# Optimization experiments

Measured on AMD Instinct MI355X. Metric: run time of the kernel, lower is better.

## Reference

```python
import jax, jax.numpy as jnp
import numpy as np

ATTRIBUTE_NUMS = [3, 3, 1, 4, 3]
WINDOW_SIZE = 10


def setup_inputs() -> dict:
    key = jax.random.key(0)
    ks = jax.random.split(key, 7)
    b, s, n_l, f = 4, 2048, 4, 64
    A, L = 14, 5  # num_attributes, levels per attribute
    scale_tensor = jax.random.normal(ks[0], (b, s, n_l, f), dtype=jnp.float32)
    scale = 1.0 / np.sqrt(f).astype(np.float32)
    Wq = jax.random.normal(ks[1], (A, L, f, f), dtype=jnp.float32) * scale
    bq = jax.random.normal(ks[2], (A, L, f), dtype=jnp.float32) * 0.01
    Wk = jax.random.normal(ks[3], (A, L, f, f), dtype=jnp.float32) * scale
    bk = jax.random.normal(ks[4], (A, L, f), dtype=jnp.float32) * 0.01
    Wt = jax.random.normal(ks[5], (A, L, f, f), dtype=jnp.float32) * scale
    bt = jax.random.normal(ks[6], (A, L, f), dtype=jnp.float32) * 0.01
    return {"scale_tensor": scale_tensor, "Wq": Wq, "bq": bq, "Wk": Wk,
            "bk": bk, "Wt": Wt, "bt": bt, "scale_idx": 4}


def reference(scale_tensor, Wq, bq, Wk, bk, Wt, bt, scale_idx):
    b, s, a, f = scale_tensor.shape
    k = WINDOW_SIZE * (6 - scale_idx)  # half window (static python int)
    w = 2 * k + 1
    l_i = scale_idx
    off = sum(ATTRIBUTE_NUMS[:scale_idx - 1])
    # select the parameters actually used: attributes [off, off+a), levels [0, l_i)
    Wq_s, bq_s = Wq[off:off + a, :l_i], bq[off:off + a, :l_i]  # [a,l,f,f], [a,l,f]
    Wk_s, bk_s = Wk[off:off + a, :l_i], bk[off:off + a, :l_i]
    Wt_s, bt_s = Wt[off:off + a, :l_i], bt[off:off + a, :l_i]

    # sliding windows over the sequence axis (zero-padded), shared across levels
    padded = jnp.pad(scale_tensor, ((0, 0), (k, k), (0, 0), (0, 0)))
    idx = jnp.arange(s)[:, None] + jnp.arange(w)[None, :]  # [s, w]
    win = padded[:, idx]                                   # [b,s,w,a,f]
    zero_mask = jnp.all(win == 0, axis=-1)                 # [b,s,w,a]

    # queries: q = x @ Wq^T + bq  (torch Linear convention, W is [out,in])
    q = jnp.einsum('bsaf,algf->bsalg', scale_tensor, Wq_s) + bq_s  # [b,s,a,l,f]
    qk = jnp.einsum('bsalg,algf->bsalf', q, Wk_s)                  # [b,s,a,l,f]
    attn = jnp.einsum('bsalf,bswaf->bsalw', qk, win)
    attn = attn + jnp.einsum('bsalg,alg->bsal', q, bk_s)[..., None]
    attn = attn / np.float32(np.sqrt(f))

    mask = jnp.transpose(zero_mask, (0, 1, 3, 2))[:, :, :, None, :]  # [b,s,a,1,w]
    attn = jnp.where(mask, jnp.float32(-1e9), attn)
    wgt = jax.nn.softmax(attn, axis=-1)                    # [b,s,a,l,w]

    ctx = jnp.einsum('bsalw,bswaf->bsalf', wgt, win)       # [b,s,a,l,f]
    out = jnp.einsum('bsalf,algf->bsalg', ctx, Wt_s) + bt_s
    return out  # [b,s,a,l_i,f]
```

## Files before the change

### kernel.cpp

```cpp
#include <hip/hip_runtime.h>
#include <hip/hip_bf16.h>

#define SDIM 2048
#define ADIM 4
#define KWIN 20
#define WWIN 41
#define CHUNK 64

typedef __attribute__((ext_vector_type(8))) short s8v;
typedef __attribute__((ext_vector_type(4))) float f32x4;
#define MFMA __builtin_amdgcn_mfma_f32_16x16x32_bf16

#define WSB_MB 8256
#define WSB_WT 172096

#define O_YJF 0
#define O_YFJ 16128
#define O_B1  31488
#define O_CTX 40704
#define O_RF  49920
#define LDS_TOTAL 50368

__device__ __forceinline__ int detect_is_bf16(const void* xp) {
  const unsigned* w = (const unsigned*)xp;
  const unsigned word = w[threadIdx.x & 63];
  const unsigned e = (word >> 7) & 0xFFu;
  const unsigned long long m = __ballot(e >= 118u && e <= 132u);
  return __popcll(m) >= 32;
}
__device__ __forceinline__ float ldf(const void* p, size_t i, int isbf) {
  return isbf ? __bfloat162float(((const __hip_bfloat16*)p)[i]) : ((const float*)p)[i];
}
__device__ __forceinline__ s8v ld8l(const char* p) { return *(const s8v*)p; }
__device__ __forceinline__ s8v ld8g(const short* p) { return *(const s8v*)p; }

__global__ __launch_bounds__(256) void prep_kernel(
    const void* __restrict__ x,
    const void* __restrict__ Wq, const void* __restrict__ bq,
    const void* __restrict__ Wk, const void* __restrict__ bk,
    const void* __restrict__ Wt, const void* __restrict__ bt,
    const int* __restrict__ sip, float* __restrict__ ws) {
  const int isbf = detect_is_bf16(x);
  const int al = blockIdx.x, a = al >> 2, li = al & 3;
  const int si = *sip;
  int off = 0;
  const int ATTR[5] = {3, 3, 1, 4, 3};
  for (int i = 0; i < si - 1 && i < 5; ++i) off += ATTR[i];
  const size_t wb = ((size_t)(off + a) * 5 + li) * 4096;
  const size_t bb = ((size_t)(off + a) * 5 + li) * 64;
  const int tid = threadIdx.x;

  __shared__ float sq[4096], sk[4096];
  __shared__ float sbq[64], sbk[64];
  for (int i = tid; i < 4096; i += 256) {
    sq[i] = ldf(Wq, wb + i, isbf);
    sk[i] = ldf(Wk, wb + i, isbf);
  }
  if (tid < 64) { sbq[tid] = ldf(bq, bb + tid, isbf); sbk[tid] = ldf(bk, bb + tid, isbf); }
  __syncthreads();

  __hip_bfloat16* mb  = (__hip_bfloat16*)((char*)ws + WSB_MB) + (size_t)al * 5120;
  __hip_bfloat16* wtb = (__hip_bfloat16*)((char*)ws + WSB_WT) + (size_t)al * 4096;

  for (int i = tid; i < 4096; i += 256) {
    const int f = i >> 6, f2 = i & 63;
    float acc = 0.f;
    #pragma unroll 16
    for (int g = 0; g < 64; ++g) acc += sk[g * 64 + f] * sq[g * 64 + f2];
    mb[f * 64 + f2] = __float2bfloat16(acc);
    wtb[i] = __float2bfloat16(ldf(Wt, wb + i, isbf));
  }
  if (tid < 64) {
    float u = 0.f, v = 0.f;
    for (int g = 0; g < 64; ++g) {
      u += sq[g * 64 + tid] * sbk[g];
      v += sk[g * 64 + tid] * sbq[g];
    }
    mb[64 * 64 + tid] = __float2bfloat16(u);
    ws[al * 64 + tid] = v;
    ws[1024 + al * 64 + tid] = ldf(bt, bb + tid, isbf);
  }
  for (int i = tid; i < 15 * 64; i += 256) mb[65 * 64 + i] = __float2bfloat16(0.f);
  if (tid == 0) {
    float c = 0.f;
    for (int g = 0; g < 64; ++g) c += sbq[g] * sbk[g];
    ws[2048 + al] = c;
  }
}

__global__ __launch_bounds__(256) void attn_kernel(
    const void* __restrict__ x, const float* __restrict__ ws,
    float* __restrict__ out) {
  const int isbf = detect_is_bf16(x);
  const int chunk = blockIdx.x;
  const int ba = blockIdx.y;
  const int b = ba >> 2, a = ba & 3;
  const int s0 = chunk * CHUNK;
  const int tid = threadIdx.x;
  const int lane = tid & 63;
  const int mt = tid >> 6;
  const int c16 = lane & 15;
  const int q = lane >> 4;

  __shared__ __align__(16) char lds[LDS_TOTAL];

  for (int r = mt; r < 112; r += 4) {
    const int j = s0 - KWIN + r;
    float yv = 0.f;
    if (r < 104 && j >= 0 && j < SDIM)
      yv = ldf(x, (((size_t)b * SDIM + j) * ADIM + a) * 64 + lane, isbf);
    const __hip_bfloat16 hv = __float2bfloat16(yv);
    *(__hip_bfloat16*)(lds + O_YJF + r * 144 + lane * 2) = hv;
    *(__hip_bfloat16*)(lds + O_YFJ + lane * 240 + r * 2) = hv;
    const unsigned long long nz = __ballot(yv != 0.f);
    if (lane == 0) ((float*)(lds + O_RF))[r] = nz ? 1.f : 0.f;
  }
  __syncthreads();

  const short* mbase  = (const short*)((const char*)ws + WSB_MB);
  const short* wtbase = (const short*)((const char*)ws + WSB_WT);

  const char* xr = lds + O_YJF + (KWIN + 16 * mt + c16) * 144 + q * 16;
  const s8v xa0 = ld8l(xr), xa1 = ld8l(xr + 64);
  float rfv[4];
  #pragma unroll
  for (int nt = 0; nt < 4; ++nt)
    rfv[nt] = ((const float*)(lds + O_RF))[16 * mt + nt * 16 + c16];

  for (int l = 0; l < 4; ++l) {
    const int al = a * 4 + l;
    const short* mb  = mbase + (size_t)al * 5120;
    const short* wtb = wtbase + (size_t)al * 4096;
    const float c_al = ws[2048 + al];

    f32x4 uacc;
    #pragma unroll
    for (int nt = 0; nt < 5; ++nt) {
      const int n = nt * 16 + c16;
      const s8v b0 = ld8g(mb + n * 64 + q * 8);
      const s8v b1 = ld8g(mb + n * 64 + 32 + q * 8);
      const float vv = (nt < 4) ? ws[al * 64 + n] : 0.f;
      f32x4 acc = {vv, vv, vv, vv};
      acc = MFMA(xa0, b0, acc, 0, 0, 0);
      acc = MFMA(xa1, b1, acc, 0, 0, 0);
      if (nt < 4) {
        #pragma unroll
        for (int r = 0; r < 4; ++r)
          *(__hip_bfloat16*)(lds + O_B1 + (16 * mt + 4 * q + r) * 144 + n * 2) =
              __float2bfloat16(acc[r]);
      } else {
        uacc = acc;
      }
    }
    float uxr[4];
    #pragma unroll
    for (int r = 0; r < 4; ++r) uxr[r] = __shfl(uacc[r], lane & 48) + c_al;
    __threadfence_block();

    const char* qrow = lds + O_B1 + (16 * mt + c16) * 144 + q * 16;
    const s8v qa0 = ld8l(qrow), qa1 = ld8l(qrow + 64);
    f32x4 sacc[4];
    #pragma unroll
    for (int nt = 0; nt < 4; ++nt) {
      const char* yr = lds + O_YJF + (16 * mt + nt * 16 + c16) * 144 + q * 16;
      const s8v b0 = ld8l(yr), b1 = ld8l(yr + 64);
      f32x4 s = {0.f, 0.f, 0.f, 0.f};
      s = MFMA(qa0, b0, s, 0, 0, 0);
      s = MFMA(qa1, b1, s, 0, 0, 0);
      sacc[nt] = s;
    }

    float ee[4][4];
    float mx[4] = {-3.0e38f, -3.0e38f, -3.0e38f, -3.0e38f};
    #pragma unroll
    for (int nt = 0; nt < 4; ++nt) {
      const int jl = nt * 16 + c16;
      #pragma unroll
      for (int r = 0; r < 4; ++r) {
        const int w = jl - (4 * q + r);
        float lv = -1.0e9f;
        if (w >= 0 && w < WWIN && rfv[nt] != 0.f)
          lv = (sacc[nt][r] + uxr[r]) * 0.125f;
        ee[nt][r] = lv;
        mx[r] = fmaxf(mx[r], lv);
      }
    }
    #pragma unroll
    for (int r = 0; r < 4; ++r) {
      #pragma unroll
      for (int o = 1; o < 16; o <<= 1) mx[r] = fmaxf(mx[r], __shfl_xor(mx[r], o));
    }
    float se[4] = {0.f, 0.f, 0.f, 0.f};
    #pragma unroll
    for (int nt = 0; nt < 4; ++nt)
      #pragma unroll
      for (int r = 0; r < 4; ++r) {
        const float e = __expf(ee[nt][r] - mx[r]);
        ee[nt][r] = e;
        se[r] += e;
      }
    float rse[4];
    #pragma unroll
    for (int r = 0; r < 4; ++r) {
      #pragma unroll
      for (int o = 1; o < 16; o <<= 1) se[r] += __shfl_xor(se[r], o);
      rse[r] = 1.f / se[r];
    }
    #pragma unroll
    for (int nt = 0; nt < 4; ++nt)
      #pragma unroll
      for (int r = 0; r < 4; ++r)
        *(__hip_bfloat16*)(lds + O_B1 + (16 * mt + 4 * q + r) * 144 +
                           (nt * 16 + c16) * 2) = __float2bfloat16(ee[nt][r]);
    __threadfence_block();

    const char* prow = lds + O_B1 + (16 * mt + c16) * 144 + q * 16;
    const s8v pa0 = ld8l(prow), pa1 = ld8l(prow + 64);
    #pragma unroll
    for (int nt = 0; nt < 4; ++nt) {
      const int f = nt * 16 + c16;
      const char* brow = lds + O_YFJ + f * 240 + 32 * mt + q * 16;
      const s8v b0 = ld8l(brow), b1 = ld8l(brow + 64);
      f32x4 cc = {0.f, 0.f, 0.f, 0.f};
      cc = MFMA(pa0, b0, cc, 0, 0, 0);
      cc = MFMA(pa1, b1, cc, 0, 0, 0);
      #pragma unroll
      for (int r = 0; r < 4; ++r)
        *(__hip_bfloat16*)(lds + O_CTX + (16 * mt + 4 * q + r) * 144 + f * 2) =
            __float2bfloat16(cc[r] * rse[r]);
    }
    __threadfence_block();

    const char* crow = lds + O_CTX + (16 * mt + c16) * 144 + q * 16;
    const s8v ca0 = ld8l(crow), ca1 = ld8l(crow + 64);
    #pragma unroll
    for (int nt = 0; nt < 4; ++nt) {
      const int g = nt * 16 + c16;
      const s8v b0 = ld8g(wtb + g * 64 + q * 8);
      const s8v b1 = ld8g(wtb + g * 64 + 32 + q * 8);
      f32x4 o = {0.f, 0.f, 0.f, 0.f};
      o = MFMA(ca0, b0, o, 0, 0, 0);
      o = MFMA(ca1, b1, o, 0, 0, 0);
      const float btv = ws[1024 + al * 64 + g];
      #pragma unroll
      for (int r = 0; r < 4; ++r) {
        const int row = 16 * mt + 4 * q + r;
        const size_t idx =
            (((size_t)b * SDIM + (s0 + row)) * ADIM + a) * 256 + l * 64 + g;
        out[idx] = o[r] + btv;
      }
    }
  }
}

extern "C" void kernel_launch(void* const* d_in, const int* in_sizes, int n_in,
                              void* d_out, int out_size, void* d_ws, size_t ws_size,
                              hipStream_t stream) {
  const void* x  = d_in[0];
  const void* Wq = d_in[1];
  const void* bq = d_in[2];
  const void* Wk = d_in[3];
  const void* bk = d_in[4];
  const void* Wt = d_in[5];
  const void* bt = d_in[6];
  const int* sip = (const int*)d_in[7];
  float* ws = (float*)d_ws;
  float* out = (float*)d_out;

  prep_kernel<<<16, 256, 0, stream>>>(x, Wq, bq, Wk, bk, Wt, bt, sip, ws);
  attn_kernel<<<dim3(SDIM / CHUNK, 16), 256, 0, stream>>>(x, ws, out);
}
```

Before: 137.2 us.

## Keep attention intermediates in registers via transposed MFMA and lane shuffles

The attention kernel swaps MFMA operand order so each result tile comes out transposed, then rebuilds the next MFMA's operand with cross-lane shuffles instead of bouncing q, probabilities and context through LDS. This removes the B1/CTX scratch regions and their LDS round-trips, cutting LDS size. It also splits levels across a new grid z-dimension for more blocks, vectorizes the input and output accesses with float4, and spreads the prep kernel over four blocks per (attribute, level). The cost is extra shuffle instructions and some duplicated x staging across the two level-halves.

```diff
diff --git a/kernel.cpp b/kernel.cpp
--- a/kernel.cpp
+++ b/kernel.cpp
@@ -2,10 +2,8 @@
 #include <hip/hip_bf16.h>
 
 #define SDIM 2048
-#define ADIM 4
 #define KWIN 20
 #define WWIN 41
-#define CHUNK 64
 
 typedef __attribute__((ext_vector_type(8))) short s8v;
 typedef __attribute__((ext_vector_type(4))) float f32x4;
@@ -16,10 +14,8 @@
 
 #define O_YJF 0
 #define O_YFJ 16128
-#define O_B1  31488
-#define O_CTX 40704
-#define O_RF  49920
-#define LDS_TOTAL 50368
+#define O_RF  31488
+#define LDS_TOTAL 31936
 
 __device__ __forceinline__ int detect_is_bf16(const void* xp) {
   const unsigned* w = (const unsigned*)xp;
@@ -31,8 +27,29 @@
 __device__ __forceinline__ float ldf(const void* p, size_t i, int isbf) {
   return isbf ? __bfloat162float(((const __hip_bfloat16*)p)[i]) : ((const float*)p)[i];
 }
-__device__ __forceinline__ s8v ld8l(const char* p) { return *(const s8v*)p; }
-__device__ __forceinline__ s8v ld8g(const short* p) { return *(const s8v*)p; }
+__device__ __forceinline__ unsigned bfb(float f) {
+  union { float f; unsigned u; } x; x.f = f;
+  return (x.u + 0x7FFFu + ((x.u >> 16) & 1u)) >> 16;
+}
+__device__ __forceinline__ int pkbf(float a, float b) {
+  return (int)(bfb(a) | (bfb(b) << 16));
+}
+__device__ __forceinline__ s8v xform(int p00, int p01, int p10, int p11, int lane) {
+  const int q = lane >> 4;
+  const int sA = (lane & 15) + ((q & 1) << 5);
+  const int sB = sA + 16;
+  const bool hi = (q >> 1) != 0;
+  const int w0a = __shfl(p00, sA), w0b = __shfl(p10, sA);
+  const int w1a = __shfl(p01, sA), w1b = __shfl(p11, sA);
+  const int w2a = __shfl(p00, sB), w2b = __shfl(p10, sB);
+  const int w3a = __shfl(p01, sB), w3b = __shfl(p11, sB);
+  union { int i[4]; s8v v; } u;
+  u.i[0] = hi ? w0b : w0a;
+  u.i[1] = hi ? w1b : w1a;
+  u.i[2] = hi ? w2b : w2a;
+  u.i[3] = hi ? w3b : w3a;
+  return u.v;
+}
 
 __global__ __launch_bounds__(256) void prep_kernel(
     const void* __restrict__ x,
@@ -42,6 +59,7 @@
     const int* __restrict__ sip, float* __restrict__ ws) {
   const int isbf = detect_is_bf16(x);
   const int al = blockIdx.x, a = al >> 2, li = al & 3;
+  const int fq = blockIdx.y;
   const int si = *sip;
   int off = 0;
   const int ATTR[5] = {3, 3, 1, 4, 3};
@@ -62,40 +80,43 @@
   __hip_bfloat16* mb  = (__hip_bfloat16*)((char*)ws + WSB_MB) + (size_t)al * 5120;
   __hip_bfloat16* wtb = (__hip_bfloat16*)((char*)ws + WSB_WT) + (size_t)al * 4096;
 
-  for (int i = tid; i < 4096; i += 256) {
-    const int f = i >> 6, f2 = i & 63;
+  for (int t = tid; t < 1024; t += 256) {
+    const int f = fq * 16 + (t >> 6), f2 = t & 63;
     float acc = 0.f;
     #pragma unroll 16
     for (int g = 0; g < 64; ++g) acc += sk[g * 64 + f] * sq[g * 64 + f2];
     mb[f * 64 + f2] = __float2bfloat16(acc);
-    wtb[i] = __float2bfloat16(ldf(Wt, wb + i, isbf));
-  }
-  if (tid < 64) {
-    float u = 0.f, v = 0.f;
-    for (int g = 0; g < 64; ++g) {
-      u += sq[g * 64 + tid] * sbk[g];
-      v += sk[g * 64 + tid] * sbq[g];
-    }
-    mb[64 * 64 + tid] = __float2bfloat16(u);
-    ws[al * 64 + tid] = v;
-    ws[1024 + al * 64 + tid] = ldf(bt, bb + tid, isbf);
-  }
-  for (int i = tid; i < 15 * 64; i += 256) mb[65 * 64 + i] = __float2bfloat16(0.f);
-  if (tid == 0) {
-    float c = 0.f;
-    for (int g = 0; g < 64; ++g) c += sbq[g] * sbk[g];
-    ws[2048 + al] = c;
-  }
-}
-
-__global__ __launch_bounds__(256) void attn_kernel(
+    wtb[f * 64 + f2] = __float2bfloat16(ldf(Wt, wb + f * 64 + f2, isbf));
+  }
+  if (fq == 0) {
+    if (tid < 64) {
+      float u = 0.f, v = 0.f;
+      for (int g = 0; g < 64; ++g) {
+        u += sq[g * 64 + tid] * sbk[g];
+        v += sk[g * 64 + tid] * sbq[g];
+      }
+      mb[64 * 64 + tid] = __float2bfloat16(u);
+      ws[al * 64 + tid] = v;
+      ws[1024 + al * 64 + tid] = ldf(bt, bb + tid, isbf);
+    }
+    for (int i = tid; i < 15 * 64; i += 256) mb[65 * 64 + i] = __float2bfloat16(0.f);
+    if (tid == 0) {
+      float c = 0.f;
+      for (int g = 0; g < 64; ++g) c += sbq[g] * sbk[g];
+      ws[2048 + al] = c;
+    }
+  }
+}
+
+__global__ __launch_bounds__(256, 4) void attn_kernel(
     const void* __restrict__ x, const float* __restrict__ ws,
     float* __restrict__ out) {
   const int isbf = detect_is_bf16(x);
   const int chunk = blockIdx.x;
   const int ba = blockIdx.y;
+  const int lp = blockIdx.z;
   const int b = ba >> 2, a = ba & 3;
-  const int s0 = chunk * CHUNK;
+  const int s0 = chunk * 64;
   const int tid = threadIdx.x;
   const int lane = tid & 63;
   const int mt = tid >> 6;
@@ -104,151 +125,149 @@
 
   __shared__ __align__(16) char lds[LDS_TOTAL];
 
-  for (int r = mt; r < 112; r += 4) {
+  #pragma unroll
+  for (int it = 0; it < 7; ++it) {
+    const int r = it * 16 + (tid >> 4);
     const int j = s0 - KWIN + r;
-    float yv = 0.f;
-    if (r < 104 && j >= 0 && j < SDIM)
-      yv = ldf(x, (((size_t)b * SDIM + j) * ADIM + a) * 64 + lane, isbf);
-    const __hip_bfloat16 hv = __float2bfloat16(yv);
-    *(__hip_bfloat16*)(lds + O_YJF + r * 144 + lane * 2) = hv;
-    *(__hip_bfloat16*)(lds + O_YFJ + lane * 240 + r * 2) = hv;
-    const unsigned long long nz = __ballot(yv != 0.f);
-    if (lane == 0) ((float*)(lds + O_RF))[r] = nz ? 1.f : 0.f;
+    float4 yv = {0.f, 0.f, 0.f, 0.f};
+    if (r < 104 && j >= 0 && j < SDIM) {
+      if (isbf) {
+        const size_t base = (((size_t)b * SDIM + j) * 4 + a) * 64 + c16 * 4;
+        yv.x = ldf(x, base, 1); yv.y = ldf(x, base + 1, 1);
+        yv.z = ldf(x, base + 2, 1); yv.w = ldf(x, base + 3, 1);
+      } else {
+        yv = *((const float4*)x + (((size_t)b * SDIM + j) * 4 + a) * 16 + c16);
+      }
+    }
+    const int f0 = c16 * 4;
+    ((int*)(lds + O_YJF + r * 144 + f0 * 2))[0] = pkbf(yv.x, yv.y);
+    ((int*)(lds + O_YJF + r * 144 + f0 * 2))[1] = pkbf(yv.z, yv.w);
+    *(unsigned short*)(lds + O_YFJ + (f0 + 0) * 240 + r * 2) = (unsigned short)bfb(yv.x);
+    *(unsigned short*)(lds + O_YFJ + (f0 + 1) * 240 + r * 2) = (unsigned short)bfb(yv.y);
+    *(unsigned short*)(lds + O_YFJ + (f0 + 2) * 240 + r * 2) = (unsigned short)bfb(yv.z);
+    *(unsigned short*)(lds + O_YFJ + (f0 + 3) * 240 + r * 2) = (unsigned short)bfb(yv.w);
+    const bool nz = (yv.x != 0.f) || (yv.y != 0.f) || (yv.z != 0.f) || (yv.w != 0.f);
+    const unsigned long long m = __ballot(nz);
+    if (c16 == 0) ((float*)(lds + O_RF))[r] = ((m >> (q * 16)) & 0xFFFFull) ? 1.f : 0.f;
   }
   __syncthreads();
 
   const short* mbase  = (const short*)((const char*)ws + WSB_MB);
   const short* wtbase = (const short*)((const char*)ws + WSB_WT);
-
-  const char* xr = lds + O_YJF + (KWIN + 16 * mt + c16) * 144 + q * 16;
-  const s8v xa0 = ld8l(xr), xa1 = ld8l(xr + 64);
-  float rfv[4];
+  const char* yjf = lds + O_YJF;
+  const char* yfj = lds + O_YFJ;
+
+  const s8v xb0 = *(const s8v*)(yjf + (KWIN + 16 * mt + c16) * 144 + 16 * q);
+  const s8v xb1 = *(const s8v*)(yjf + (KWIN + 16 * mt + c16) * 144 + 64 + 16 * q);
+  float rfarr[16];
   #pragma unroll
-  for (int nt = 0; nt < 4; ++nt)
-    rfv[nt] = ((const float*)(lds + O_RF))[16 * mt + nt * 16 + c16];
-
-  for (int l = 0; l < 4; ++l) {
+  for (int nt = 0; nt < 4; ++nt) {
+    const float4 t = *(const float4*)((const float*)(lds + O_RF) + 16 * mt + 16 * nt + 4 * q);
+    rfarr[nt * 4 + 0] = t.x; rfarr[nt * 4 + 1] = t.y;
+    rfarr[nt * 4 + 2] = t.z; rfarr[nt * 4 + 3] = t.w;
+  }
+
+  for (int li = 0; li < 2; ++li) {
+    const int l = lp * 2 + li;
     const int al = a * 4 + l;
     const short* mb  = mbase + (size_t)al * 5120;
     const short* wtb = wtbase + (size_t)al * 4096;
     const float c_al = ws[2048 + al];
 
-    f32x4 uacc;
+    int pq[4][2];
+    f32x4 uacc = {0.f, 0.f, 0.f, 0.f};
     #pragma unroll
     for (int nt = 0; nt < 5; ++nt) {
-      const int n = nt * 16 + c16;
-      const s8v b0 = ld8g(mb + n * 64 + q * 8);
-      const s8v b1 = ld8g(mb + n * 64 + 32 + q * 8);
-      const float vv = (nt < 4) ? ws[al * 64 + n] : 0.f;
-      f32x4 acc = {vv, vv, vv, vv};
-      acc = MFMA(xa0, b0, acc, 0, 0, 0);
-      acc = MFMA(xa1, b1, acc, 0, 0, 0);
+      const int rowm = (nt < 4) ? (16 * nt + c16) : (64 + c16);
+      const s8v a0 = *(const s8v*)(mb + rowm * 64 + 8 * q);
+      const s8v a1 = *(const s8v*)(mb + rowm * 64 + 32 + 8 * q);
+      f32x4 acc;
       if (nt < 4) {
-        #pragma unroll
-        for (int r = 0; r < 4; ++r)
-          *(__hip_bfloat16*)(lds + O_B1 + (16 * mt + 4 * q + r) * 144 + n * 2) =
-              __float2bfloat16(acc[r]);
+        const float4 v4 = *(const float4*)(ws + al * 64 + 16 * nt + 4 * q);
+        acc[0] = v4.x; acc[1] = v4.y; acc[2] = v4.z; acc[3] = v4.w;
       } else {
-        uacc = acc;
-      }
-    }
-    float uxr[4];
-    #pragma unroll
-    for (int r = 0; r < 4; ++r) uxr[r] = __shfl(uacc[r], lane & 48) + c_al;
-    __threadfence_block();
-
-    const char* qrow = lds + O_B1 + (16 * mt + c16) * 144 + q * 16;
-    const s8v qa0 = ld8l(qrow), qa1 = ld8l(qrow + 64);
-    f32x4 sacc[4];
-    #pragma unroll
-    for (int nt = 0; nt < 4; ++nt) {
-      const char* yr = lds + O_YJF + (16 * mt + nt * 16 + c16) * 144 + q * 16;
-      const s8v b0 = ld8l(yr), b1 = ld8l(yr + 64);
+        acc[0] = acc[1] = acc[2] = acc[3] = 0.f;
+      }
+      acc = MFMA(a0, xb0, acc, 0, 0, 0);
+      acc = MFMA(a1, xb1, acc, 0, 0, 0);
+      if (nt < 4) { pq[nt][0] = pkbf(acc[0], acc[1]); pq[nt][1] = pkbf(acc[2], acc[3]); }
+      else uacc = acc;
+    }
+    const float ux = __shfl(uacc[0], lane & 15) + c_al;
+    const s8v qb0 = xform(pq[0][0], pq[0][1], pq[1][0], pq[1][1], lane);
+    const s8v qb1 = xform(pq[2][0], pq[2][1], pq[3][0], pq[3][1], lane);
+
+    f32x4 st[4];
+    #pragma unroll
+    for (int nt = 0; nt < 4; ++nt) {
+      const char* yr = yjf + (16 * mt + 16 * nt + c16) * 144 + 16 * q;
+      const s8v a0 = *(const s8v*)yr;
+      const s8v a1 = *(const s8v*)(yr + 64);
       f32x4 s = {0.f, 0.f, 0.f, 0.f};
-      s = MFMA(qa0, b0, s, 0, 0, 0);
-      s = MFMA(qa1, b1, s, 0, 0, 0);
-      sacc[nt] = s;
-    }
-
-    float ee[4][4];
-    float mx[4] = {-3.0e38f, -3.0e38f, -3.0e38f, -3.0e38f};
-    #pragma unroll
-    for (int nt = 0; nt < 4; ++nt) {
-      const int jl = nt * 16 + c16;
-      #pragma unroll
-      for (int r = 0; r < 4; ++r) {
-        const int w = jl - (4 * q + r);
-        float lv = -1.0e9f;
-        if (w >= 0 && w < WWIN && rfv[nt] != 0.f)
-          lv = (sacc[nt][r] + uxr[r]) * 0.125f;
-        ee[nt][r] = lv;
-        mx[r] = fmaxf(mx[r], lv);
-      }
-    }
-    #pragma unroll
-    for (int r = 0; r < 4; ++r) {
-      #pragma unroll
-      for (int o = 1; o < 16; o <<= 1) mx[r] = fmaxf(mx[r], __shfl_xor(mx[r], o));
-    }
-    float se[4] = {0.f, 0.f, 0.f, 0.f};
+      s = MFMA(a0, qb0, s, 0, 0, 0);
+      s = MFMA(a1, qb1, s, 0, 0, 0);
+      st[nt] = s;
+    }
+
+    float ee[16];
+    float mx = -3.0e38f;
     #pragma unroll
     for (int nt = 0; nt < 4; ++nt)
       #pragma unroll
       for (int r = 0; r < 4; ++r) {
-        const float e = __expf(ee[nt][r] - mx[r]);
-        ee[nt][r] = e;
-        se[r] += e;
-      }
-    float rse[4];
-    #pragma unroll
-    for (int r = 0; r < 4; ++r) {
-      #pragma unroll
-      for (int o = 1; o < 16; o <<= 1) se[r] += __shfl_xor(se[r], o);
-      rse[r] = 1.f / se[r];
-    }
-    #pragma unroll
-    for (int nt = 0; nt < 4; ++nt)
-      #pragma unroll
-      for (int r = 0; r < 4; ++r)
-        *(__hip_bfloat16*)(lds + O_B1 + (16 * mt + 4 * q + r) * 144 +
-                           (nt * 16 + c16) * 2) = __float2bfloat16(ee[nt][r]);
-    __threadfence_block();
-
-    const char* prow = lds + O_B1 + (16 * mt + c16) * 144 + q * 16;
-    const s8v pa0 = ld8l(prow), pa1 = ld8l(prow + 64);
-    #pragma unroll
-    for (int nt = 0; nt < 4; ++nt) {
-      const int f = nt * 16 + c16;
-      const char* brow = lds + O_YFJ + f * 240 + 32 * mt + q * 16;
-      const s8v b0 = ld8l(brow), b1 = ld8l(brow + 64);
+        const int w = 16 * nt + 4 * q + r - c16;
+        float lv = -1.0e9f;
+        if (w >= 0 && w < WWIN && rfarr[nt * 4 + r] != 0.f)
+          lv = (st[nt][r] + ux) * 0.125f;
+        ee[nt * 4 + r] = lv;
+        mx = fmaxf(mx, lv);
+      }
+    mx = fmaxf(mx, __shfl_xor(mx, 16));
+    mx = fmaxf(mx, __shfl_xor(mx, 32));
+    float se = 0.f;
+    #pragma unroll
+    for (int i = 0; i < 16; ++i) { ee[i] = __expf(ee[i] - mx); se += ee[i]; }
+    se += __shfl_xor(se, 16);
+    se += __shfl_xor(se, 32);
+    const float rse = 1.f / se;
+
+    int pp[4][2];
+    #pragma unroll
+    for (int nt = 0; nt < 4; ++nt) {
+      pp[nt][0] = pkbf(ee[nt * 4 + 0], ee[nt * 4 + 1]);
+      pp[nt][1] = pkbf(ee[nt * 4 + 2], ee[nt * 4 + 3]);
+    }
+    const s8v pb0 = xform(pp[0][0], pp[0][1], pp[1][0], pp[1][1], lane);
+    const s8v pb1 = xform(pp[2][0], pp[2][1], pp[3][0], pp[3][1], lane);
+
+    int cp[4][2];
+    #pragma unroll
+    for (int nt = 0; nt < 4; ++nt) {
+      const char* fr = yfj + (16 * nt + c16) * 240 + 32 * mt + 16 * q;
+      const s8v a0 = *(const s8v*)fr;
+      const s8v a1 = *(const s8v*)(fr + 64);
       f32x4 cc = {0.f, 0.f, 0.f, 0.f};
-      cc = MFMA(pa0, b0, cc, 0, 0, 0);
-      cc = MFMA(pa1, b1, cc, 0, 0, 0);
-      #pragma unroll
-      for (int r = 0; r < 4; ++r)
-        *(__hip_bfloat16*)(lds + O_CTX + (16 * mt + 4 * q + r) * 144 + f * 2) =
-            __float2bfloat16(cc[r] * rse[r]);
-    }
-    __threadfence_block();
-
-    const char* crow = lds + O_CTX + (16 * mt + c16) * 144 + q * 16;
-    const s8v ca0 = ld8l(crow), ca1 = ld8l(crow + 64);
-    #pragma unroll
-    for (int nt = 0; nt < 4; ++nt) {
-      const int g = nt * 16 + c16;
-      const s8v b0 = ld8g(wtb + g * 64 + q * 8);
-      const s8v b1 = ld8g(wtb + g * 64 + 32 + q * 8);
-      f32x4 o = {0.f, 0.f, 0.f, 0.f};
-      o = MFMA(ca0, b0, o, 0, 0, 0);
-      o = MFMA(ca1, b1, o, 0, 0, 0);
-      const float btv = ws[1024 + al * 64 + g];
-      #pragma unroll
-      for (int r = 0; r < 4; ++r) {
-        const int row = 16 * mt + 4 * q + r;
-        const size_t idx =
-            (((size_t)b * SDIM + (s0 + row)) * ADIM + a) * 256 + l * 64 + g;
-        out[idx] = o[r] + btv;
-      }
+      cc = MFMA(a0, pb0, cc, 0, 0, 0);
+      cc = MFMA(a1, pb1, cc, 0, 0, 0);
+      cp[nt][0] = pkbf(cc[0] * rse, cc[1] * rse);
+      cp[nt][1] = pkbf(cc[2] * rse, cc[3] * rse);
+    }
+    const s8v cb0 = xform(cp[0][0], cp[0][1], cp[1][0], cp[1][1], lane);
+    const s8v cb1 = xform(cp[2][0], cp[2][1], cp[3][0], cp[3][1], lane);
+
+    const int row = 16 * mt + c16;
+    float* obase = out + ((((size_t)b * SDIM + s0 + row) * 4 + a) * 4 + l) * 64 + 4 * q;
+    #pragma unroll
+    for (int nt = 0; nt < 4; ++nt) {
+      const s8v a0 = *(const s8v*)(wtb + (16 * nt + c16) * 64 + 8 * q);
+      const s8v a1 = *(const s8v*)(wtb + (16 * nt + c16) * 64 + 32 + 8 * q);
+      const float4 b4 = *(const float4*)(ws + 1024 + al * 64 + 16 * nt + 4 * q);
+      f32x4 o;
+      o[0] = b4.x; o[1] = b4.y; o[2] = b4.z; o[3] = b4.w;
+      o = MFMA(a0, cb0, o, 0, 0, 0);
+      o = MFMA(a1, cb1, o, 0, 0, 0);
+      float4 o4; o4.x = o[0]; o4.y = o[1]; o4.z = o[2]; o4.w = o[3];
+      *(float4*)(obase + 16 * nt) = o4;
     }
   }
 }
@@ -267,6 +286,6 @@
   float* ws = (float*)d_ws;
   float* out = (float*)d_out;
 
-  prep_kernel<<<16, 256, 0, stream>>>(x, Wq, bq, Wk, bk, Wt, bt, sip, ws);
-  attn_kernel<<<dim3(SDIM / CHUNK, 16), 256, 0, stream>>>(x, ws, out);
-}
+  prep_kernel<<<dim3(16, 4), 256, 0, stream>>>(x, Wq, bq, Wk, bk, Wt, bt, sip, ws);
+  attn_kernel<<<dim3(32, 16, 2), 256, 0, stream>>>(x, ws, out);
+}
```

New measurement: 118.7 us. 13.5% less time.
